# Kernel optimization log

Measured on AMD Instinct MI355X. Metric: run time of the kernel, lower is better.

Reference implementation:

```python
import jax, jax.numpy as jnp
import numpy as np

N = 50000      # nodes
E = 800000     # edges before self loops
D = 64         # hidden dim (num_heads = 1)
T = 2          # edge types for GatedGraphConv
STEPS = 2      # GRU propagation steps
NEG = 0.2      # leaky_relu negative slope (DGL GATv2Conv default)


def setup_inputs() -> dict:
    key = jax.random.key(0)
    ks = jax.random.split(key, 40)
    s = 1.0 / np.sqrt(D)
    inp = {
        "x": jax.random.normal(ks[0], (N, D), jnp.float32),
        "src": jax.random.randint(ks[1], (E,), 0, N),
        "dst": jax.random.randint(ks[2], (E,), 0, N),
        "etypes": jax.random.randint(ks[3], (E + N,), 0, T),
    }
    i = 4
    for l in range(2):
        inp[f"gat{l}_Wsrc"] = jax.random.normal(ks[i], (D, D), jnp.float32) * s; i += 1
        inp[f"gat{l}_bsrc"] = jnp.zeros((D,), jnp.float32)
        inp[f"gat{l}_Wdst"] = jax.random.normal(ks[i], (D, D), jnp.float32) * s; i += 1
        inp[f"gat{l}_bdst"] = jnp.zeros((D,), jnp.float32)
        inp[f"gat{l}_attn"] = jax.random.normal(ks[i], (D,), jnp.float32) * s; i += 1
        inp[f"ggc{l}_W"] = jax.random.normal(ks[i], (T, D, D), jnp.float32) * s; i += 1
        inp[f"ggc{l}_b"] = jnp.zeros((T, D), jnp.float32)
        inp[f"ggc{l}_Wih"] = jax.random.normal(ks[i], (3 * D, D), jnp.float32) * s; i += 1
        inp[f"ggc{l}_bih"] = jnp.zeros((3 * D,), jnp.float32)
        inp[f"ggc{l}_Whh"] = jax.random.normal(ks[i], (3 * D, D), jnp.float32) * s; i += 1
        inp[f"ggc{l}_bhh"] = jnp.zeros((3 * D,), jnp.float32)
    return inp


def _gatv2(x, Wsrc, bsrc, Wdst, bdst, attn, srcF, dstF):
    # DGL GATv2Conv, 1 head, feat_drop=attn_drop=0, residual=False, activation=elu
    el = x @ Wsrc.T + bsrc                            # (N, D)
    er = x @ Wdst.T + bdst                            # (N, D)
    e = jax.nn.leaky_relu(el[srcF] + er[dstF], NEG)   # (Ef, D)
    score = e @ attn                                  # (Ef,)
    m = jax.ops.segment_max(score, dstF, num_segments=N)
    ex = jnp.exp(score - m[dstF])
    den = jax.ops.segment_sum(ex, dstF, num_segments=N)
    a = ex / den[dstF]                                # edge softmax over incoming edges
    out = jax.ops.segment_sum(a[:, None] * el[srcF], dstF, num_segments=N)
    return jax.nn.elu(out)


def _ggc(h, W, b, Wih, bih, Whh, bhh, srcF, dstF, etypes):
    # DGL GatedGraphConv: per-etype linear on source feats, sum-aggregate, GRUCell
    for _ in range(STEPS):
        trans = jnp.einsum("nd,tod->tno", h, W) + b[:, None, :]  # (T, N, D)
        msg = trans[etypes, srcF]                                # (Ef, D)
        a = jax.ops.segment_sum(msg, dstF, num_segments=N)       # (N, D)
        gi = a @ Wih.T + bih
        gh = h @ Whh.T + bhh
        ir, iz, ic = jnp.split(gi, 3, -1)
        hr, hz, hc = jnp.split(gh, 3, -1)
        r = jax.nn.sigmoid(ir + hr)
        z = jax.nn.sigmoid(iz + hz)
        c = jnp.tanh(ic + r * hc)
        h = (1.0 - z) * c + z * h
    return h


def reference(x, src, dst, etypes,
              gat0_Wsrc, gat0_bsrc, gat0_Wdst, gat0_bdst, gat0_attn,
              ggc0_W, ggc0_b, ggc0_Wih, ggc0_bih, ggc0_Whh, ggc0_bhh,
              gat1_Wsrc, gat1_bsrc, gat1_Wdst, gat1_bdst, gat1_attn,
              ggc1_W, ggc1_b, ggc1_Wih, ggc1_bih, ggc1_Whh, ggc1_bhh):
    loops = jnp.arange(N, dtype=src.dtype)
    srcF = jnp.concatenate([src, loops])  # dgl.add_self_loop
    dstF = jnp.concatenate([dst, loops])
    gat = [(gat0_Wsrc, gat0_bsrc, gat0_Wdst, gat0_bdst, gat0_attn),
           (gat1_Wsrc, gat1_bsrc, gat1_Wdst, gat1_bdst, gat1_attn)]
    ggc = [(ggc0_W, ggc0_b, ggc0_Wih, ggc0_bih, ggc0_Whh, ggc0_bhh),
           (ggc1_W, ggc1_b, ggc1_Wih, ggc1_bih, ggc1_Whh, ggc1_bhh)]
    emb = []
    feats = x
    for l in range(2):
        feats = _gatv2(feats, *gat[l], srcF, dstF)
        emb.append(feats)
        feats = _ggc(feats, *ggc[l], srcF, dstF, etypes)
        emb.append(feats)
    return jnp.stack(emb)  # (4, N, D) == embedding list of the torch module
```

## Files before the change

kernel.cpp:

```cpp
#include <hip/hip_runtime.h>
#include <math.h>

#define NN 50000
#define EE 800000
#define EF (EE + NN)
#define DD 64
#define NEG_SLOPE 0.2f
#define NT16 3125
#define NN2 (2 * NN)

#define BSHIFT 8
#define NPB 256
#define NB 196
#define CAP 6144
#define PTILE 4096
#define NPBLK ((EF + PTILE - 1) / PTILE)

#define WPK_WF    16384
#define WPK_TOTAL (88 * 1024)

typedef unsigned short ushort;
typedef __attribute__((ext_vector_type(8))) short short8;
typedef __attribute__((ext_vector_type(4))) float floatx4;
typedef __attribute__((ext_vector_type(4))) unsigned int uintx4;

union frag_u { uintx4 u; short8 s; };

__device__ __forceinline__ ushort f2bf(float f) {
  union { float f; unsigned u; } v; v.f = f;
  unsigned r = v.u + 0x7FFFu + ((v.u >> 16) & 1u);
  return (ushort)(r >> 16);
}
__device__ __forceinline__ float bf2f(ushort h) {
  union { unsigned u; float f; } v; v.u = ((unsigned)h) << 16;
  return v.f;
}

__device__ __forceinline__ void split8v(float4 f0, float4 f1, short8& hi, short8& lo) {
  float v[8] = {f0.x, f0.y, f0.z, f0.w, f1.x, f1.y, f1.z, f1.w};
#pragma unroll
  for (int j = 0; j < 8; j++) {
    ushort h = f2bf(v[j]);
    hi[j] = (short)h;
    lo[j] = (short)f2bf(v[j] - bf2f(h));
  }
}

__device__ __forceinline__ void split8(const float* __restrict__ p, short8& hi, short8& lo) {
  float4 f0 = *(const float4*)p;
  float4 f1 = *(const float4*)(p + 4);
  split8v(f0, f1, hi, lo);
}


__global__ void k_zero(int* __restrict__ p, int n) {
  int i = blockIdx.x * blockDim.x + threadIdx.x;
  if (i < n) p[i] = 0;
}

__global__ __launch_bounds__(256) void k_part(
    const int* __restrict__ src, const int* __restrict__ dst,
    const int* __restrict__ etypes,
    int* __restrict__ cursorB, int* __restrict__ pairbuf) {
  __shared__ int hist[NB];
  __shared__ int excl[NB];
  __shared__ int resv[NB];
  __shared__ int stmp[256];
  __shared__ int sbuf[PTILE];
  __shared__ int sdst[PTILE];
  int tid = threadIdx.x;
  int e0 = blockIdx.x * PTILE;
  int cnt = EF - e0; if (cnt > PTILE) cnt = PTILE;

  if (tid < NB) hist[tid] = 0;
  __syncthreads();

  int val[16], bk[16], rk[16];
#pragma unroll
  for (int j = 0; j < 16; j++) {
    int e = e0 + j * 256 + tid;
    bk[j] = -1;
    if (e < EF) {
      int d = (e < EE) ? dst[e] : (e - EE);
      int s = (e < EE) ? src[e] : (e - EE);
      int t = etypes[e];
      int b = d >> BSHIFT;
      val[j] = ((((d & (NPB - 1)) << 1) | t) << 16) | s;
      bk[j] = b;
      rk[j] = atomicAdd(&hist[b], 1);
    }
  }
  __syncthreads();

  stmp[tid] = (tid < NB) ? hist[tid] : 0;
  __syncthreads();
#pragma unroll
  for (int off = 1; off < 256; off <<= 1) {
    int t = (tid >= off) ? stmp[tid - off] : 0;
    __syncthreads();
    stmp[tid] += t;
    __syncthreads();
  }
  if (tid < NB) {
    excl[tid] = stmp[tid] - hist[tid];
    resv[tid] = atomicAdd(&cursorB[tid], hist[tid]);
  }
  __syncthreads();

#pragma unroll
  for (int j = 0; j < 16; j++) {
    if (bk[j] >= 0) {
      int o = excl[bk[j]] + rk[j];
      sbuf[o] = val[j];
      sdst[o] = bk[j] * CAP + resv[bk[j]] + rk[j];
    }
  }
  __syncthreads();

  for (int i = tid; i < cnt; i += 256) {
    pairbuf[sdst[i]] = sbuf[i];
  }
}

__global__ __launch_bounds__(256) void k_build(
    const int* __restrict__ cursorB, const int* __restrict__ pairbuf,
    int* __restrict__ rs2, int* __restrict__ csr_s) {
  __shared__ int sa[512];
  __shared__ int sb[512];
  __shared__ int stage[CAP];
  __shared__ int s_base;
  int tid = threadIdx.x;
  int b = blockIdx.x;

  sa[tid] = (tid < NB) ? cursorB[tid] : 0;
  __syncthreads();
#pragma unroll
  for (int off = 1; off < 256; off <<= 1) {
    int t = (tid >= off) ? sa[tid - off] : 0;
    __syncthreads();
    sa[tid] += t;
    __syncthreads();
  }
  if (tid == 0) s_base = (b > 0) ? sa[b - 1] : 0;
  __syncthreads();
  int base = s_base;
  int cnt = cursorB[b];

  for (int s = tid; s < 512; s += 256) sa[s] = 0;
  __syncthreads();
  const int* pb = pairbuf + b * CAP;
  for (int i = tid; i < cnt; i += 256) {
    atomicAdd(&sa[pb[i] >> 16], 1);
  }
  __syncthreads();

  int* A = sa; int* B = sb;
#pragma unroll
  for (int off = 1; off < 512; off <<= 1) {
    for (int s = tid; s < 512; s += 256) {
      B[s] = A[s] + ((s >= off) ? A[s - off] : 0);
    }
    __syncthreads();
    int* t = A; A = B; B = t;
  }

  for (int s = tid; s < 512; s += 256) {
    int ex = (s > 0) ? A[s - 1] : 0;
    B[s] = ex;
    int idx = (b << 9) + s;
    if (idx <= NN2) rs2[idx] = base + ex;
  }
  __syncthreads();

  for (int i = tid; i < cnt; i += 256) {
    int v = pb[i];
    int p = atomicAdd(&B[v >> 16], 1);
    stage[p] = v & 0xFFFF;
  }
  __syncthreads();

  for (int i = tid; i < cnt; i += 256) {
    csr_s[base + i] = stage[i];
  }
}


__global__ void k_combine(const float* __restrict__ Wih, const float* __restrict__ gW,
                          const float* __restrict__ gb,
                          float* __restrict__ Wcfp, float* __restrict__ bvec) {
  int idx = blockIdx.x * 256 + threadIdx.x;
  if (idx < 2 * 192 * 64) {
    int t = idx / (192 * 64);
    int rem = idx - t * (192 * 64);
    int c = rem >> 6, k = rem & 63;
    const float* wr = Wih + c * 64;
    const float* wc = gW + t * 64 * 64 + k;
    float s = 0.f;
#pragma unroll 8
    for (int j = 0; j < 64; j++) s += wr[j] * wc[j * 64];
    Wcfp[idx] = s;
  } else if (idx < 2 * 192 * 64 + 384) {
    int f = idx - 2 * 192 * 64;
    int t = f / 192, c = f - t * 192;
    const float* wr = Wih + c * 64;
    const float* bb = gb + t * 64;
    float s = 0.f;
#pragma unroll 8
    for (int j = 0; j < 64; j++) s += bb[j] * wr[j];
    bvec[f] = s;
  }
}

__global__ void k_split_w(const float* __restrict__ Wsrc, const float* __restrict__ Wdst,
                          const float* __restrict__ Wcfp, const float* __restrict__ Whh,
                          ushort* __restrict__ wpk) {
  int t = blockIdx.x * 256 + threadIdx.x;
  if (t >= 88 * 64) return;
  int frag = t >> 6, lane = t & 63;
  int nloc = lane & 15, q = lane >> 4;
  float v[8];
  if (frag < 16) {
    int mat = frag >> 3;
    int nt = (frag >> 1) & 3;
    int ks = frag & 1;
    const float* W = mat ? Wdst : Wsrc;
    const float* row = W + (nt * 16 + nloc) * 64 + ks * 32 + q * 8;
#pragma unroll
    for (int j = 0; j < 8; j++) v[j] = row[j];
  } else {
    int f = frag - 16;
    int nt = f & 3;
    int gg = (f >> 2) % 3;
    int ks = f / 12;
    int c = gg * 64 + nt * 16 + nloc;
    int k0 = ks * 32 + q * 8;
#pragma unroll
    for (int j = 0; j < 8; j++) {
      int kk = k0 + j;
      v[j] = (kk < 64) ? Wcfp[c * 64 + kk]
           : (kk < 128) ? Wcfp[192 * 64 + c * 64 + (kk - 64)]
                        : Whh[c * 64 + (kk - 128)];
    }
  }
  ushort* d = wpk + (size_t)frag * 1024 + lane * 16;
#pragma unroll
  for (int j = 0; j < 8; j++) {
    ushort h = f2bf(v[j]);
    d[j] = h;
    d[8 + j] = f2bf(v[j] - bf2f(h));
  }
}


__global__ __launch_bounds__(256) void k_linear2_mfma(
    const float* __restrict__ x, const ushort* __restrict__ wpk,
    const float* __restrict__ bsrc, const float* __restrict__ bdst,
    float* __restrict__ el, float* __restrict__ er) {
  int tid = threadIdx.x;
  int lane = tid & 63;
  int wid = tid >> 6;
  int mat = wid & 1, nh = wid >> 1;
  int tile = blockIdx.x;
  int nloc = lane & 15, q = lane >> 4;

  floatx4 acc[2];
  acc[0] = (floatx4)0.f; acc[1] = (floatx4)0.f;

#pragma unroll
  for (int ks = 0; ks < 2; ks++) {
    const float* ap = x + (size_t)(tile * 16 + nloc) * DD + ks * 32 + q * 8;
    short8 ah, al;
    split8(ap, ah, al);
#pragma unroll
    for (int j = 0; j < 2; j++) {
      int nt = nh * 2 + j;
      const ushort* bp = wpk + ((size_t)((mat * 4 + nt) * 2 + ks)) * 1024 + lane * 16;
      frag_u bh, bl;
      bh.u = *(const uintx4*)bp;
      bl.u = *(const uintx4*)(bp + 8);
      acc[j] = __builtin_amdgcn_mfma_f32_16x16x32_bf16(ah, bh.s, acc[j], 0, 0, 0);
      acc[j] = __builtin_amdgcn_mfma_f32_16x16x32_bf16(ah, bl.s, acc[j], 0, 0, 0);
      acc[j] = __builtin_amdgcn_mfma_f32_16x16x32_bf16(al, bh.s, acc[j], 0, 0, 0);
    }
  }

  float* outp = mat ? er : el;
  const float* bb = mat ? bdst : bsrc;
#pragma unroll
  for (int j = 0; j < 2; j++) {
    int col = (nh * 2 + j) * 16 + nloc;
    float b0 = bb[col];
#pragma unroll
    for (int r = 0; r < 4; r++) {
      int row = tile * 16 + q * 4 + r;
      outp[(size_t)row * DD + col] = acc[j][r] + b0;
    }
  }
}

__global__ __launch_bounds__(256) void k_gat_fused(
    const float* __restrict__ el, const float* __restrict__ er,
    const float* __restrict__ attn,
    const int* __restrict__ rs2, const int* __restrict__ csr_s,
    float* __restrict__ out) {
  int lane = threadIdx.x & 63;
  int n = blockIdx.x * 4 + (threadIdx.x >> 6);
  if (n >= NN) return;
  int r0 = rs2[2 * n], r1 = rs2[2 * n + 2];
  int eg = lane >> 4, c4 = lane & 15;
  const float4* el4 = (const float4*)el;
  float4 erv = ((const float4*)er)[(size_t)n * 16 + c4];
  float4 at4 = ((const float4*)attn)[c4];

  float d = 0.f;
  float ax = 0.f, ay = 0.f, az = 0.f, aw = 0.f;
  for (int i = r0 + eg; i < r1; i += 4) {
    int s = csr_s[i];
    float4 v = el4[(size_t)s * 16 + c4];
    float p, t;
    t = v.x + erv.x; t = fmaxf(t, NEG_SLOPE * t); p = t * at4.x;
    t = v.y + erv.y; t = fmaxf(t, NEG_SLOPE * t); p = fmaf(t, at4.y, p);
    t = v.z + erv.z; t = fmaxf(t, NEG_SLOPE * t); p = fmaf(t, at4.z, p);
    t = v.w + erv.w; t = fmaxf(t, NEG_SLOPE * t); p = fmaf(t, at4.w, p);
#pragma unroll
    for (int off = 1; off <= 8; off <<= 1) p += __shfl_xor(p, off, 64);
    float w = __expf(p);
    d += w;
    ax = fmaf(w, v.x, ax);
    ay = fmaf(w, v.y, ay);
    az = fmaf(w, v.z, az);
    aw = fmaf(w, v.w, aw);
  }
#pragma unroll
  for (int off = 16; off <= 32; off <<= 1) {
    d  += __shfl_xor(d, off, 64);
    ax += __shfl_xor(ax, off, 64);
    ay += __shfl_xor(ay, off, 64);
    az += __shfl_xor(az, off, 64);
    aw += __shfl_xor(aw, off, 64);
  }
  if (eg == 0) {
    float inv = 1.f / d;
    float4 o;
    o.x = ax * inv; o.y = ay * inv; o.z = az * inv; o.w = aw * inv;
    o.x = (o.x > 0.f) ? o.x : expm1f(o.x);
    o.y = (o.y > 0.f) ? o.y : expm1f(o.y);
    o.z = (o.z > 0.f) ? o.z : expm1f(o.z);
    o.w = (o.w > 0.f) ? o.w : expm1f(o.w);
    ((float4*)out)[(size_t)n * 16 + c4] = o;
  }
}


__device__ __forceinline__ void gsum(const float4* __restrict__ h4,
                                     const int* __restrict__ csr_s,
                                     int lo, int hi, int eg, int c4,
                                     float& rx, float& ry, float& rz, float& rw) {
  float x0 = 0.f, y0 = 0.f, z0 = 0.f, w0 = 0.f;
  float x1 = 0.f, y1 = 0.f, z1 = 0.f, w1 = 0.f;
  for (int i = lo; i < hi; i += 8) {
    int e0 = i + eg, e1 = i + 4 + eg;
    if (e0 < hi) {
      float4 v = h4[(size_t)csr_s[e0] * 16 + c4];
      x0 += v.x; y0 += v.y; z0 += v.z; w0 += v.w;
    }
    if (e1 < hi) {
      float4 v = h4[(size_t)csr_s[e1] * 16 + c4];
      x1 += v.x; y1 += v.y; z1 += v.z; w1 += v.w;
    }
  }
  rx = x0 + x1; ry = y0 + y1; rz = z0 + z1; rw = w0 + w1;
}

__global__ __launch_bounds__(256) void k_ggc_fused(
    const float* __restrict__ h_in,
    const ushort* __restrict__ wpk,
    const float* __restrict__ bih, const float* __restrict__ bhh,
    const float* __restrict__ bvec,
    const int* __restrict__ rs2, const int* __restrict__ csr_s,
    float* __restrict__ h_out) {
  __shared__ float lsS[2][16][68];
  int tid = threadIdx.x;
  int lane = tid & 63;
  int wid = tid >> 6;
  int tile = blockIdx.x;
  int eg = lane >> 4, c4 = lane & 15;
  const float4* h4 = (const float4*)h_in;

#pragma unroll
  for (int k = 0; k < 4; k++) {
    int nl = (wid << 2) + k;
    int n = tile * 16 + nl;
    int r0 = rs2[2 * n], rsp = rs2[2 * n + 1], r1 = rs2[2 * n + 2];
    float t0x, t0y, t0z, t0w, t1x, t1y, t1z, t1w;
    gsum(h4, csr_s, r0, rsp, eg, c4, t0x, t0y, t0z, t0w);
    gsum(h4, csr_s, rsp, r1, eg, c4, t1x, t1y, t1z, t1w);
#pragma unroll
    for (int off = 16; off <= 32; off <<= 1) {
      t0x += __shfl_xor(t0x, off, 64); t0y += __shfl_xor(t0y, off, 64);
      t0z += __shfl_xor(t0z, off, 64); t0w += __shfl_xor(t0w, off, 64);
      t1x += __shfl_xor(t1x, off, 64); t1y += __shfl_xor(t1y, off, 64);
      t1z += __shfl_xor(t1z, off, 64); t1w += __shfl_xor(t1w, off, 64);
    }
    if (eg == 0) {
      float* p0 = &lsS[0][nl][c4 * 4];
      p0[0] = t0x; p0[1] = t0y; p0[2] = t0z; p0[3] = t0w;
      float* p1 = &lsS[1][nl][c4 * 4];
      p1[0] = t1x; p1[1] = t1y; p1[2] = t1z; p1[3] = t1w;
    }
  }
  __syncthreads();

  int nt = wid;
  int nloc = lane & 15, q = lane >> 4;
  const ushort* wf = wpk + WPK_WF;

  floatx4 ar = (floatx4)0.f, az = (floatx4)0.f;
  floatx4 aic = (floatx4)0.f, ahc = (floatx4)0.f;

#pragma unroll
  for (int ks = 0; ks < 6; ks++) {
    float4 f0, f1;
    if (ks < 4) {
      const float* ap = &lsS[ks >> 1][nloc][(ks & 1) * 32 + q * 8];
      f0 = *(const float4*)ap;
      f1 = *(const float4*)(ap + 4);
    } else {
      const float* ap = h_in + (size_t)(tile * 16 + nloc) * DD + (ks & 1) * 32 + q * 8;
      f0 = *(const float4*)ap;
      f1 = *(const float4*)(ap + 4);
    }
    short8 fah, fal;
    split8v(f0, f1, fah, fal);
#pragma unroll
    for (int g = 0; g < 3; g++) {
      const ushort* bp = wf + ((size_t)((ks * 3 + g) * 4 + nt)) * 1024 + lane * 16;
      frag_u bh, bl;
      bh.u = *(const uintx4*)bp;
      bl.u = *(const uintx4*)(bp + 8);
      floatx4* acc = (g == 0) ? &ar : (g == 1) ? &az : ((ks < 4) ? &aic : &ahc);
      *acc = __builtin_amdgcn_mfma_f32_16x16x32_bf16(fah, bh.s, *acc, 0, 0, 0);
      *acc = __builtin_amdgcn_mfma_f32_16x16x32_bf16(fah, bl.s, *acc, 0, 0, 0);
      *acc = __builtin_amdgcn_mfma_f32_16x16x32_bf16(fal, bh.s, *acc, 0, 0, 0);
    }
  }

  int col = nt * 16 + nloc;
  float bvr0 = bvec[col], bvz0 = bvec[64 + col], bvc0 = bvec[128 + col];
  float bvr1 = bvec[192 + col], bvz1 = bvec[256 + col], bvc1 = bvec[320 + col];
  float br = bih[col] + bhh[col];
  float bz = bih[64 + col] + bhh[64 + col];
  float bic = bih[128 + col], bhc = bhh[128 + col];
#pragma unroll
  for (int r = 0; r < 4; r++) {
    int row = tile * 16 + q * 4 + r;
    int ra = rs2[2 * row], rb = rs2[2 * row + 1], rc = rs2[2 * row + 2];
    float c0v = (float)(rb - ra), c1v = (float)(rc - rb);
    float rr = 1.f / (1.f + expf(-(ar[r] + br + c0v * bvr0 + c1v * bvr1)));
    float zz = 1.f / (1.f + expf(-(az[r] + bz + c0v * bvz0 + c1v * bvz1)));
    float icv = aic[r] + bic + c0v * bvc0 + c1v * bvc1;
    float hcv = ahc[r] + bhc;
    float cc = tanhf(icv + rr * hcv);
    float hp = h_in[(size_t)row * DD + col];
    h_out[(size_t)row * DD + col] = (1.f - zz) * cc + zz * hp;
  }
}


extern "C" void kernel_launch(void* const* d_in, const int* in_sizes, int n_in,
                              void* d_out, int out_size, void* d_ws, size_t ws_size,
                              hipStream_t stream) {
  const float* x = (const float*)d_in[0];
  const int* src = (const int*)d_in[1];
  const int* dst = (const int*)d_in[2];
  const int* etypes = (const int*)d_in[3];

  float* out = (float*)d_out;

  float* el = (float*)d_ws;
  float* er = el + (size_t)NN * DD;
  float* big = er + (size_t)NN * DD;
  float* htmp = el;
  float* Wcfp = big + (size_t)2 * NN * DD;
  float* bvec = Wcfp + 2 * 192 * 64;
  ushort* wpk = (ushort*)(bvec + 2 * 384);
  int* cursorB = (int*)(wpk + 2 * WPK_TOTAL);
  int* rs2 = cursorB + NB;
  int* csr_s = rs2 + (NN2 + 1);
  int* pairbuf = csr_s + EF;

  k_zero<<<1, 256, 0, stream>>>(cursorB, NB);
  k_part<<<NPBLK, 256, 0, stream>>>(src, dst, etypes, cursorB, pairbuf);
  k_build<<<NB, 256, 0, stream>>>(cursorB, pairbuf, rs2, csr_s);

  for (int l = 0; l < 2; l++) {
    int base = 4 + 11 * l;
    k_combine<<<98, 256, 0, stream>>>(
        (const float*)d_in[base + 7], (const float*)d_in[base + 5],
        (const float*)d_in[base + 6], Wcfp, bvec + l * 384);
    k_split_w<<<22, 256, 0, stream>>>(
        (const float*)d_in[base + 0], (const float*)d_in[base + 2],
        Wcfp, (const float*)d_in[base + 9], wpk + (size_t)l * WPK_TOTAL);
  }

  for (int l = 0; l < 2; l++) {
    int base = 4 + 11 * l;
    const float* bsrc = (const float*)d_in[base + 1];
    const float* bdst = (const float*)d_in[base + 3];
    const float* attn = (const float*)d_in[base + 4];
    const float* bih  = (const float*)d_in[base + 8];
    const float* bhh  = (const float*)d_in[base + 10];
    const ushort* lwpk = wpk + (size_t)l * WPK_TOTAL;
    const float* lbvec = bvec + l * 384;

    const float* xin = (l == 0) ? x : (out + 1 * (size_t)NN * DD);
    float* emb_gat = out + (size_t)(2 * l) * NN * DD;
    float* emb_ggc = out + (size_t)(2 * l + 1) * NN * DD;

    k_linear2_mfma<<<NT16, 256, 0, stream>>>(xin, lwpk, bsrc, bdst, el, er);
    k_gat_fused<<<(NN + 3) / 4, 256, 0, stream>>>(el, er, attn, rs2, csr_s, emb_gat);

    k_ggc_fused<<<NT16, 256, 0, stream>>>(emb_gat, lwpk, bih, bhh, lbvec,
                                          rs2, csr_s, htmp);

    k_ggc_fused<<<NT16, 256, 0, stream>>>(htmp, lwpk, bih, bhh, lbvec,
                                          rs2, csr_s, emb_ggc);
  }
}
```

Before: 514.5 us.

## Stage tile CSR indices in LDS and reassign GGC neighbour gather per segment

The fused GGC kernel now copies each tile's CSR source indices and row starts into shared memory once. Each 16-lane group then sums one (node, edge-type) segment with an 8-way unrolled loop, replacing the earlier scheme where 4 lane groups split each segment and combined results with cross-lane shuffles. The aim is more gathers in flight per thread, fewer global index loads and no shuffle reduction. Separately, expf and tanhf in the GRU epilogue are replaced with fast __expf-based forms, which trades a little accuracy for fewer instructions. The fixed 1024-entry index buffer assumes no 16-node tile has more than 1024 incoming edges.

```diff
diff --git a/kernel.cpp b/kernel.cpp
--- a/kernel.cpp
+++ b/kernel.cpp
@@ -351,26 +351,7 @@
   }
 }
 
-
-__device__ __forceinline__ void gsum(const float4* __restrict__ h4,
-                                     const int* __restrict__ csr_s,
-                                     int lo, int hi, int eg, int c4,
-                                     float& rx, float& ry, float& rz, float& rw) {
-  float x0 = 0.f, y0 = 0.f, z0 = 0.f, w0 = 0.f;
-  float x1 = 0.f, y1 = 0.f, z1 = 0.f, w1 = 0.f;
-  for (int i = lo; i < hi; i += 8) {
-    int e0 = i + eg, e1 = i + 4 + eg;
-    if (e0 < hi) {
-      float4 v = h4[(size_t)csr_s[e0] * 16 + c4];
-      x0 += v.x; y0 += v.y; z0 += v.z; w0 += v.w;
-    }
-    if (e1 < hi) {
-      float4 v = h4[(size_t)csr_s[e1] * 16 + c4];
-      x1 += v.x; y1 += v.y; z1 += v.z; w1 += v.w;
-    }
-  }
-  rx = x0 + x1; ry = y0 + y1; rz = z0 + z1; rw = w0 + w1;
-}
+#define TEC 1024
 
 __global__ __launch_bounds__(256) void k_ggc_fused(
     const float* __restrict__ h_in,
@@ -380,33 +361,62 @@
     const int* __restrict__ rs2, const int* __restrict__ csr_s,
     float* __restrict__ h_out) {
   __shared__ float lsS[2][16][68];
+  __shared__ int sidx[TEC];
+  __shared__ int srs[33];
   int tid = threadIdx.x;
   int lane = tid & 63;
   int wid = tid >> 6;
   int tile = blockIdx.x;
-  int eg = lane >> 4, c4 = lane & 15;
   const float4* h4 = (const float4*)h_in;
 
-#pragma unroll
-  for (int k = 0; k < 4; k++) {
-    int nl = (wid << 2) + k;
-    int n = tile * 16 + nl;
-    int r0 = rs2[2 * n], rsp = rs2[2 * n + 1], r1 = rs2[2 * n + 2];
-    float t0x, t0y, t0z, t0w, t1x, t1y, t1z, t1w;
-    gsum(h4, csr_s, r0, rsp, eg, c4, t0x, t0y, t0z, t0w);
-    gsum(h4, csr_s, rsp, r1, eg, c4, t1x, t1y, t1z, t1w);
-#pragma unroll
-    for (int off = 16; off <= 32; off <<= 1) {
-      t0x += __shfl_xor(t0x, off, 64); t0y += __shfl_xor(t0y, off, 64);
-      t0z += __shfl_xor(t0z, off, 64); t0w += __shfl_xor(t0w, off, 64);
-      t1x += __shfl_xor(t1x, off, 64); t1y += __shfl_xor(t1y, off, 64);
-      t1z += __shfl_xor(t1z, off, 64); t1w += __shfl_xor(t1w, off, 64);
-    }
-    if (eg == 0) {
-      float* p0 = &lsS[0][nl][c4 * 4];
-      p0[0] = t0x; p0[1] = t0y; p0[2] = t0z; p0[3] = t0w;
-      float* p1 = &lsS[1][nl][c4 * 4];
-      p1[0] = t1x; p1[1] = t1y; p1[2] = t1z; p1[3] = t1w;
+  int R0 = rs2[tile * 32];
+  int tcnt = rs2[tile * 32 + 32] - R0;
+  if (tid < 33) srs[tid] = rs2[tile * 32 + tid];
+  for (int i = tid; i < tcnt; i += 256) sidx[i] = csr_s[R0 + i];
+  __syncthreads();
+
+  {
+    int q = tid & 15;
+#pragma unroll
+    for (int pass = 0; pass < 2; pass++) {
+      int s = (tid >> 4) + pass * 16;
+      int lo = srs[s] - R0, hi = srs[s + 1] - R0;
+      float ax = 0.f, ay = 0.f, az = 0.f, aw = 0.f;
+      for (int i = lo; i < hi; i += 8) {
+        {
+          float4 v = h4[(size_t)sidx[i] * 16 + q];
+          ax += v.x; ay += v.y; az += v.z; aw += v.w;
+        }
+        if (i + 1 < hi) {
+          float4 v = h4[(size_t)sidx[i + 1] * 16 + q];
+          ax += v.x; ay += v.y; az += v.z; aw += v.w;
+        }
+        if (i + 2 < hi) {
+          float4 v = h4[(size_t)sidx[i + 2] * 16 + q];
+          ax += v.x; ay += v.y; az += v.z; aw += v.w;
+        }
+        if (i + 3 < hi) {
+          float4 v = h4[(size_t)sidx[i + 3] * 16 + q];
+          ax += v.x; ay += v.y; az += v.z; aw += v.w;
+        }
+        if (i + 4 < hi) {
+          float4 v = h4[(size_t)sidx[i + 4] * 16 + q];
+          ax += v.x; ay += v.y; az += v.z; aw += v.w;
+        }
+        if (i + 5 < hi) {
+          float4 v = h4[(size_t)sidx[i + 5] * 16 + q];
+          ax += v.x; ay += v.y; az += v.z; aw += v.w;
+        }
+        if (i + 6 < hi) {
+          float4 v = h4[(size_t)sidx[i + 6] * 16 + q];
+          ax += v.x; ay += v.y; az += v.z; aw += v.w;
+        }
+        if (i + 7 < hi) {
+          float4 v = h4[(size_t)sidx[i + 7] * 16 + q];
+          ax += v.x; ay += v.y; az += v.z; aw += v.w;
+        }
+      }
+      *(float4*)&lsS[s & 1][s >> 1][q * 4] = make_float4(ax, ay, az, aw);
     }
   }
   __syncthreads();
@@ -453,14 +463,17 @@
   float bic = bih[128 + col], bhc = bhh[128 + col];
 #pragma unroll
   for (int r = 0; r < 4; r++) {
-    int row = tile * 16 + q * 4 + r;
-    int ra = rs2[2 * row], rb = rs2[2 * row + 1], rc = rs2[2 * row + 2];
+    int rl = q * 4 + r;
+    int row = tile * 16 + rl;
+    int ra = srs[2 * rl], rb = srs[2 * rl + 1], rc = srs[2 * rl + 2];
     float c0v = (float)(rb - ra), c1v = (float)(rc - rb);
-    float rr = 1.f / (1.f + expf(-(ar[r] + br + c0v * bvr0 + c1v * bvr1)));
-    float zz = 1.f / (1.f + expf(-(az[r] + bz + c0v * bvz0 + c1v * bvz1)));
+    float rr = 1.f / (1.f + __expf(-(ar[r] + br + c0v * bvr0 + c1v * bvr1)));
+    float zz = 1.f / (1.f + __expf(-(az[r] + bz + c0v * bvz0 + c1v * bvz1)));
     float icv = aic[r] + bic + c0v * bvc0 + c1v * bvc1;
     float hcv = ahc[r] + bhc;
-    float cc = tanhf(icv + rr * hcv);
+    float xx = icv + rr * hcv;
+    float e2 = __expf(2.f * xx);
+    float cc = 1.f - 2.f / (e2 + 1.f);
     float hp = h_in[(size_t)row * DD + col];
     h_out[(size_t)row * DD + col] = (1.f - zz) * cc + zz * hp;
   }
```

Result: faster. 478.2 us (-7.1%).
